# Kernel optimization log

Hardware: AMD Instinct MI355X
Metric: run time of the kernel (lower is better)

## Reference

```python
import jax, jax.numpy as jnp
import numpy as np

N = 8192
F_DIM = 512
H_DIM = 256


def _xavier(key, shape):
    fan_in, fan_out = shape
    limit = float(np.sqrt(6.0 / (fan_in + fan_out)))
    return jax.random.uniform(key, shape, jnp.float32, -limit, limit)


def setup_inputs() -> dict:
    key = jax.random.key(0)
    k1, k2, k3, k4, k5, k6, k7 = jax.random.split(key, 7)
    inp = {
        "input": jax.random.normal(k1, (N, F_DIM), jnp.float32),
        "wavelets": jax.random.normal(k2, (N, N), jnp.float32) / np.sqrt(N),
        "wavelets_inv": jax.random.normal(k3, (N, N), jnp.float32) / np.sqrt(N),
        "W1": _xavier(k4, (F_DIM, H_DIM)),
        "W2": _xavier(k5, (H_DIM, H_DIM)),
        "filter1": jax.random.uniform(k6, (N,), jnp.float32, 0.9, 1.1),
        "filter2": jax.random.uniform(k7, (N,), jnp.float32, 0.9, 1.1),
    }
    return inp


def _gwnn_layer(x, wavelets, wavelets_inv, weight, filt):
    # torch: wavelets @ diag(filt) @ (wavelets_inv @ (x @ W))
    # diag(filt) right-multiply == column-wise scale of wavelets (same math,
    # avoids the O(N^3) dense diag matmul).
    t = x @ weight                      # [N, C_out]
    s = wavelets_inv @ t                # [N, C_out] (spectral domain)
    return (wavelets * filt[None, :]) @ s  # [N, C_out]


def reference(input, wavelets, wavelets_inv, W1, W2, filter1, filter2):
    # eval mode: dropout is identity
    h1 = jax.nn.relu(_gwnn_layer(input, wavelets, wavelets_inv, W1, filter1))
    out = _gwnn_layer(h1, wavelets, wavelets_inv, W2, filter2)
    return out
```

## Files before the change

kernel.cpp:

```cpp
#include <hip/hip_runtime.h>
#include <hip/hip_bf16.h>

using f32x4 = __attribute__((ext_vector_type(4))) float;
using s16x8 = __attribute__((ext_vector_type(8))) short;

#define DEVFN static __device__ __forceinline__

static constexpr int NCOL = 256;
static constexpr int MROWS = 8192;
static constexpr int BM = 64;
static constexpr int BK = 64;
static constexpr int THREADS = 512;
static constexpr int NTILE = MROWS / BM;
static constexpr size_t PSLICE = (size_t)MROWS * NCOL;

DEVFN unsigned short f2bf(float f) {
  union { float f; unsigned u; } x; x.f = f;
  unsigned u = x.u;
  u += 0x7fffu + ((u >> 16) & 1u);
  return (unsigned short)(u >> 16);
}

DEVFN float bf2f(unsigned short u) {
  union { unsigned u; float f; } x; x.u = (unsigned)u << 16; return x.f;
}

DEVFN s16x8 pack8(f32x4 v0, f32x4 v1) {
  union { s16x8 v; __hip_bfloat162 h[4]; } pk;
  pk.h[0] = __float22bfloat162_rn(float2{v0[0], v0[1]});
  pk.h[1] = __float22bfloat162_rn(float2{v0[2], v0[3]});
  pk.h[2] = __float22bfloat162_rn(float2{v1[0], v1[1]});
  pk.h[3] = __float22bfloat162_rn(float2{v1[2], v1[3]});
  return pk.v;
}

DEVFN void async16(void* lds, const void* g) {
  __builtin_amdgcn_global_load_lds((const __attribute__((address_space(1))) unsigned*)g,
                                   (__attribute__((address_space(3))) unsigned*)lds,
                                   16, 0, 0);
}


template<int KS>
__global__ __launch_bounds__(THREADS, 4)
void gemm_b(const unsigned short* __restrict__ Ablk, int Kfull,
            const unsigned short* __restrict__ Bp8,
            unsigned short* __restrict__ Pout)
{
  __shared__ __align__(16) unsigned short As[2][BM * BK];
  __shared__ __align__(16) unsigned short Bs[2][BK * NCOL];

  const int nwg = NTILE * KS, q = nwg / 8;
  const int logical = (blockIdx.x & 7) * q + (blockIdx.x >> 3);
  const int kh = logical / NTILE;
  const int tile = logical % NTILE;
  const int klen = Kfull / KS;
  const int nt = klen / BK;
  const int k0 = kh * klen;
  const int KT = Kfull >> 6;
  const int tid = threadIdx.x, lane = tid & 63;
  const int wm = (tid >> 6) >> 2;
  const int wn = (tid >> 6) & 3;
  const int lr = lane & 15, lg = lane >> 4;

  auto stage = [&](int buf, int t) {
    const unsigned short* asrc = Ablk + ((size_t)tile * KT + (k0 >> 6) + t) * 4096 + tid * 8;
    async16(&As[buf][tid * 8], asrc);
    const unsigned short* bsrc = Bp8 + (size_t)(k0 + t * BK) * NCOL + tid * 8;
#pragma unroll
    for (int o = 0; o < 4; ++o)
      async16(&Bs[buf][o * 4096 + tid * 8], bsrc + o * 4096);
  };

  f32x4 acc[2][4] = {};

  stage(0, 0);

  int cur = 0;
  for (int t = 0; t < nt; ++t) {
    if (t + 1 < nt) {
      stage(cur ^ 1, t + 1);
      asm volatile("s_waitcnt vmcnt(5)");
    } else {
      asm volatile("s_waitcnt vmcnt(0)");
    }
    __builtin_amdgcn_s_barrier();
    __builtin_amdgcn_sched_barrier(0);
#pragma unroll
    for (int s = 0; s < 2; ++s) {
      const int kc = s * 4 + lg;
      const int r0 = wm * 32 + lr, r1 = r0 + 16;
      s16x8 a0 = *(const s16x8*)&As[cur][r0 * 64 + ((kc ^ (r0 & 7)) << 3)];
      s16x8 a1 = *(const s16x8*)&As[cur][r1 * 64 + ((kc ^ (r1 & 7)) << 3)];
#pragma unroll
      for (int fn = 0; fn < 4; ++fn) {
        s16x8 b = *(const s16x8*)&Bs[cur][kc * 2048 + (wn * 64 + fn * 16 + lr) * 8];
        acc[0][fn] = __builtin_amdgcn_mfma_f32_16x16x32_bf16(a0, b, acc[0][fn], 0, 0, 0);
        acc[1][fn] = __builtin_amdgcn_mfma_f32_16x16x32_bf16(a1, b, acc[1][fn], 0, 0, 0);
      }
    }
    __builtin_amdgcn_s_barrier();
    cur ^= 1;
  }

  unsigned short* dst = Pout + (size_t)kh * PSLICE;
#pragma unroll
  for (int fm = 0; fm < 2; ++fm) {
    const int r0 = tile * BM + wm * 32 + fm * 16 + lg * 4;
#pragma unroll
    for (int fn = 0; fn < 4; ++fn) {
      const int col = wn * 64 + fn * 16 + lr;
      ushort4 u;
      u.x = f2bf(acc[fm][fn][0]); u.y = f2bf(acc[fm][fn][1]);
      u.z = f2bf(acc[fm][fn][2]); u.w = f2bf(acc[fm][fn][3]);
      *(ushort4*)&dst[((size_t)(r0 >> 3) * 256 + col) * 8 + (r0 & 7)] = u;
    }
  }
}


template<int KTSH>
__global__ void k_cvt_ablk(const float* __restrict__ W, unsigned short* __restrict__ outp) {
  const int K = 64 << KTSH;
  size_t gid = (size_t)blockIdx.x * blockDim.x + threadIdx.x;
  const int k8 = (int)(gid & 7);
  const size_t rr = gid >> 3;
  const int row = (int)(rr & 63);
  const size_t bt = rr >> 6;
  const int t = (int)(bt & ((1 << KTSH) - 1));
  const size_t T = bt >> KTSH;
  const float* p = W + (T * 64 + row) * (size_t)K + t * 64 + k8 * 8;
  s16x8 v = pack8(*(const f32x4*)p, *(const f32x4*)(p + 4));
  *(s16x8*)&outp[bt * 4096 + row * 64 + ((k8 ^ (row & 7)) << 3)] = v;
}

__global__ void k_convert_p8(const float* __restrict__ W, int K,
                             unsigned short* __restrict__ outp) {
  int tid = blockIdx.x * blockDim.x + threadIdx.x;
  if (tid >= K * NCOL / 4) return;
  int j = tid & (NCOL - 1);
  int i0 = (tid >> 8) << 2;
  unsigned short u[4];
#pragma unroll
  for (int r = 0; r < 4; ++r) u[r] = f2bf(W[(size_t)(i0 + r) * NCOL + j]);
  size_t off = ((size_t)(i0 >> 3) * NCOL + j) * 8 + (i0 & 7);
  *(ushort4*)&outp[off] = make_ushort4(u[0], u[1], u[2], u[3]);
}

template<int MODE>
__global__ void k_reduce(const unsigned short* __restrict__ P,
                         const float* __restrict__ filt, void* __restrict__ Out) {
  const int tid = blockIdx.x * blockDim.x + threadIdx.x;
  const int j = tid & 255;
  const int i8 = tid >> 8;
  const int i0 = i8 * 8;
  const size_t base = ((size_t)i8 * 256 + j) * 8;
  s16x8 p0 = *(const s16x8*)&P[base];
  s16x8 p1 = *(const s16x8*)&P[base + PSLICE];
  s16x8 p2 = *(const s16x8*)&P[base + 2 * PSLICE];
  s16x8 p3 = *(const s16x8*)&P[base + 3 * PSLICE];
  float f[8];
#pragma unroll
  for (int r = 0; r < 8; ++r)
    f[r] = bf2f((unsigned short)p0[r]) + bf2f((unsigned short)p1[r])
         + bf2f((unsigned short)p2[r]) + bf2f((unsigned short)p3[r]);
  if constexpr (MODE == 0) {
    if (filt) {
#pragma unroll
      for (int r = 0; r < 8; ++r) f[r] *= filt[i0 + r];
    }
    union { s16x8 v; unsigned short u[8]; } o;
#pragma unroll
    for (int r = 0; r < 8; ++r) o.u[r] = f2bf(f[r]);
    *(s16x8*)&((unsigned short*)Out)[base] = o.v;
  } else if constexpr (MODE == 1) {
    unsigned short* O = (unsigned short*)Out;
#pragma unroll
    for (int r = 0; r < 8; ++r) {
      const int row = i0 + r;
      O[((size_t)(row >> 6) * 4 + (j >> 6)) * 4096 + (row & 63) * 64
        + ((((j >> 3) & 7) ^ (row & 7)) << 3) + (j & 7)] = f2bf(fmaxf(f[r], 0.f));
    }
  } else {
    float* O = (float*)Out;
#pragma unroll
    for (int r = 0; r < 8; ++r)
      O[(size_t)(i0 + r) * NCOL + j] = f[r];
  }
}

extern "C" void kernel_launch(void* const* d_in, const int* in_sizes, int n_in,
                              void* d_out, int out_size, void* d_ws, size_t ws_size,
                              hipStream_t stream) {
  const float* input = (const float*)d_in[0];
  const float* Wv    = (const float*)d_in[1];
  const float* Winv  = (const float*)d_in[2];
  const float* W1    = (const float*)d_in[3];
  const float* W2    = (const float*)d_in[4];
  const float* f1    = (const float*)d_in[5];
  const float* f2    = (const float*)d_in[6];
  float* out = (float*)d_out;

  char* ws = (char*)d_ws;
  unsigned short* WvB   = (unsigned short*)(ws);
  unsigned short* WinvB = (unsigned short*)(ws + 0x8000000);
  unsigned short* inB   = (unsigned short*)(ws + 0x10000000);
  unsigned short* partB = (unsigned short*)(ws + 0x10800000);
  unsigned short* t1p   = (unsigned short*)(ws + 0x11800000);
  unsigned short* s1p   = (unsigned short*)(ws + 0x11C00000);
  unsigned short* t2p   = (unsigned short*)(ws + 0x12000000);
  unsigned short* s2p   = (unsigned short*)(ws + 0x12400000);
  unsigned short* h1b   = (unsigned short*)(ws + 0x12800000);
  unsigned short* W1p   = (unsigned short*)(ws + 0x12C00000);
  unsigned short* W2p   = (unsigned short*)(ws + 0x12C40000);

  dim3 gT(THREADS);
  dim3 g4(NTILE * 4), g1(NTILE);
  dim3 rT(256), rG(MROWS * NCOL / 8 / 256);

  k_cvt_ablk<7><<<dim3(32768), rT, 0, stream>>>(Wv, WvB);
  k_cvt_ablk<7><<<dim3(32768), rT, 0, stream>>>(Winv, WinvB);
  k_cvt_ablk<3><<<dim3(2048),  rT, 0, stream>>>(input, inB);
  k_convert_p8<<<dim3(128), rT, 0, stream>>>(W1, 512, W1p);
  k_convert_p8<<<dim3(64),  rT, 0, stream>>>(W2, 256, W2p);

  gemm_b<1><<<g1, gT, 0, stream>>>(inB, 512, W1p, t1p);
  gemm_b<4><<<g4, gT, 0, stream>>>(WinvB, 8192, t1p, partB);
  k_reduce<0><<<rG, rT, 0, stream>>>(partB, f1, s1p);
  gemm_b<4><<<g4, gT, 0, stream>>>(WvB, 8192, s1p, partB);
  k_reduce<1><<<rG, rT, 0, stream>>>(partB, nullptr, h1b);
  gemm_b<1><<<g1, gT, 0, stream>>>(h1b, 256, W2p, t2p);
  gemm_b<4><<<g4, gT, 0, stream>>>(WinvB, 8192, t2p, partB);
  k_reduce<0><<<rG, rT, 0, stream>>>(partB, f2, s2p);
  gemm_b<4><<<g4, gT, 0, stream>>>(WvB, 8192, s2p, partB);
  k_reduce<2><<<rG, rT, 0, stream>>>(partB, nullptr, out);
}
```

Before: 386.6 us.

## Fuse fp32-to-bf16 conversion of wavelet matrices into first-layer GEMMs with writeback

Removes the standalone conversion kernels for the wavelet matrices and the input. The first-layer GEMMs load fp32 A tiles, pack them to bf16 in registers, store them to LDS, and write the bf16 tile to the workspace for reuse by the second layer. This avoids one full extra read of each large matrix but replaces async LDS loads with register-staged loads in those GEMMs. The A LDS layout is changed to a k-chunk-major layout without XOR swizzle, which may introduce bank conflicts.

```diff
diff --git a/kernel.cpp b/kernel.cpp
--- a/kernel.cpp
+++ b/kernel.cpp
@@ -41,14 +41,15 @@
 }
 
 
-template<int KS>
+template<bool AF32, bool WB, int KS>
 __global__ __launch_bounds__(THREADS, 4)
-void gemm_b(const unsigned short* __restrict__ Ablk, int Kfull,
+void gemm_f(const void* __restrict__ Aany, int Kfull,
             const unsigned short* __restrict__ Bp8,
-            unsigned short* __restrict__ Pout)
+            unsigned short* __restrict__ Pout,
+            unsigned short* __restrict__ Awb)
 {
-  __shared__ __align__(16) unsigned short As[2][BM * BK];
-  __shared__ __align__(16) unsigned short Bs[2][BK * NCOL];
+  __shared__ __align__(16) unsigned short As[2][4096];
+  __shared__ __align__(16) unsigned short Bs[2][16384];
 
   const int nwg = NTILE * KS, q = nwg / 8;
   const int logical = (blockIdx.x & 7) * q + (blockIdx.x >> 3);
@@ -58,46 +59,84 @@
   const int nt = klen / BK;
   const int k0 = kh * klen;
   const int KT = Kfull >> 6;
+  const int kt0 = k0 >> 6;
   const int tid = threadIdx.x, lane = tid & 63;
   const int wm = (tid >> 6) >> 2;
   const int wn = (tid >> 6) & 3;
   const int lr = lane & 15, lg = lane >> 4;
-
-  auto stage = [&](int buf, int t) {
-    const unsigned short* asrc = Ablk + ((size_t)tile * KT + (k0 >> 6) + t) * 4096 + tid * 8;
-    async16(&As[buf][tid * 8], asrc);
-    const unsigned short* bsrc = Bp8 + (size_t)(k0 + t * BK) * NCOL + tid * 8;
+  const int srow = tid >> 3, sk8 = tid & 7;
+
+  auto stageB = [&](int buf, int t) {
+    const unsigned short* b = Bp8 + (size_t)(k0 + t * BK) * 256 + tid * 8;
 #pragma unroll
     for (int o = 0; o < 4; ++o)
-      async16(&Bs[buf][o * 4096 + tid * 8], bsrc + o * 4096);
+      async16(&Bs[buf][o * 4096 + tid * 8], b + o * 4096);
+  };
+  auto stageA_bf = [&](int buf, int t) {
+    async16(&As[buf][tid * 8],
+            (const unsigned short*)Aany + ((size_t)tile * KT + kt0 + t) * 4096 + tid * 8);
+  };
+
+  f32x4 ra0, ra1;
+  auto loadA = [&](int t) {
+    const float* p = (const float*)Aany + (size_t)(tile * BM + srow) * Kfull
+                   + k0 + t * BK + sk8 * 8;
+    ra0 = *(const f32x4*)p; ra1 = *(const f32x4*)(p + 4);
+  };
+  auto putA = [&](int buf, int t) {
+    s16x8 v = pack8(ra0, ra1);
+    *(s16x8*)&As[buf][sk8 * 512 + srow * 8] = v;
+    if constexpr (WB)
+      *(s16x8*)&Awb[((size_t)tile * KT + kt0 + t) * 4096 + sk8 * 512 + srow * 8] = v;
   };
 
   f32x4 acc[2][4] = {};
 
-  stage(0, 0);
+  if constexpr (AF32) {
+    loadA(0); stageB(0, 0); putA(0, 0);
+    asm volatile("s_waitcnt lgkmcnt(0)");
+  } else {
+    stageA_bf(0, 0); stageB(0, 0);
+  }
 
   int cur = 0;
   for (int t = 0; t < nt; ++t) {
-    if (t + 1 < nt) {
-      stage(cur ^ 1, t + 1);
-      asm volatile("s_waitcnt vmcnt(5)");
+    if constexpr (AF32) {
+      if (t + 1 < nt) {
+        loadA(t + 1);
+        stageB(cur ^ 1, t + 1);
+        if constexpr (WB) asm volatile("s_waitcnt vmcnt(7)");
+        else              asm volatile("s_waitcnt vmcnt(6)");
+      } else {
+        asm volatile("s_waitcnt vmcnt(0)");
+      }
     } else {
-      asm volatile("s_waitcnt vmcnt(0)");
+      if (t + 1 < nt) {
+        stageA_bf(cur ^ 1, t + 1); stageB(cur ^ 1, t + 1);
+        asm volatile("s_waitcnt vmcnt(5)");
+      } else {
+        asm volatile("s_waitcnt vmcnt(0)");
+      }
     }
     __builtin_amdgcn_s_barrier();
     __builtin_amdgcn_sched_barrier(0);
 #pragma unroll
     for (int s = 0; s < 2; ++s) {
       const int kc = s * 4 + lg;
-      const int r0 = wm * 32 + lr, r1 = r0 + 16;
-      s16x8 a0 = *(const s16x8*)&As[cur][r0 * 64 + ((kc ^ (r0 & 7)) << 3)];
-      s16x8 a1 = *(const s16x8*)&As[cur][r1 * 64 + ((kc ^ (r1 & 7)) << 3)];
+      s16x8 a0 = *(const s16x8*)&As[cur][kc * 512 + (wm * 32 + lr) * 8];
+      s16x8 a1 = *(const s16x8*)&As[cur][kc * 512 + (wm * 32 + 16 + lr) * 8];
 #pragma unroll
       for (int fn = 0; fn < 4; ++fn) {
         s16x8 b = *(const s16x8*)&Bs[cur][kc * 2048 + (wn * 64 + fn * 16 + lr) * 8];
         acc[0][fn] = __builtin_amdgcn_mfma_f32_16x16x32_bf16(a0, b, acc[0][fn], 0, 0, 0);
         acc[1][fn] = __builtin_amdgcn_mfma_f32_16x16x32_bf16(a1, b, acc[1][fn], 0, 0, 0);
       }
+    }
+    if constexpr (AF32) {
+      __builtin_amdgcn_sched_barrier(0);
+      if (t + 1 < nt) putA(cur ^ 1, t + 1);
+      asm volatile("s_waitcnt lgkmcnt(0)");
+      __builtin_amdgcn_sched_barrier(0);
     }
     __builtin_amdgcn_s_barrier();
     cur ^= 1;
@@ -118,21 +157,6 @@
   }
 }
 
-
-template<int KTSH>
-__global__ void k_cvt_ablk(const float* __restrict__ W, unsigned short* __restrict__ outp) {
-  const int K = 64 << KTSH;
-  size_t gid = (size_t)blockIdx.x * blockDim.x + threadIdx.x;
-  const int k8 = (int)(gid & 7);
-  const size_t rr = gid >> 3;
-  const int row = (int)(rr & 63);
-  const size_t bt = rr >> 6;
-  const int t = (int)(bt & ((1 << KTSH) - 1));
-  const size_t T = bt >> KTSH;
-  const float* p = W + (T * 64 + row) * (size_t)K + t * 64 + k8 * 8;
-  s16x8 v = pack8(*(const f32x4*)p, *(const f32x4*)(p + 4));
-  *(s16x8*)&outp[bt * 4096 + row * 64 + ((k8 ^ (row & 7)) << 3)] = v;
-}
 
 __global__ void k_convert_p8(const float* __restrict__ W, int K,
                              unsigned short* __restrict__ outp) {
@@ -155,15 +179,13 @@
   const int i8 = tid >> 8;
   const int i0 = i8 * 8;
   const size_t base = ((size_t)i8 * 256 + j) * 8;
-  s16x8 p0 = *(const s16x8*)&P[base];
-  s16x8 p1 = *(const s16x8*)&P[base + PSLICE];
-  s16x8 p2 = *(const s16x8*)&P[base + 2 * PSLICE];
-  s16x8 p3 = *(const s16x8*)&P[base + 3 * PSLICE];
-  float f[8];
-#pragma unroll
-  for (int r = 0; r < 8; ++r)
-    f[r] = bf2f((unsigned short)p0[r]) + bf2f((unsigned short)p1[r])
-         + bf2f((unsigned short)p2[r]) + bf2f((unsigned short)p3[r]);
+  float f[8] = {};
+#pragma unroll
+  for (int h = 0; h < 4; ++h) {
+    s16x8 pv = *(const s16x8*)&P[base + (size_t)h * PSLICE];
+#pragma unroll
+    for (int r = 0; r < 8; ++r) f[r] += bf2f((unsigned short)pv[r]);
+  }
   if constexpr (MODE == 0) {
     if (filt) {
 #pragma unroll
@@ -178,8 +200,8 @@
 #pragma unroll
     for (int r = 0; r < 8; ++r) {
       const int row = i0 + r;
-      O[((size_t)(row >> 6) * 4 + (j >> 6)) * 4096 + (row & 63) * 64
-        + ((((j >> 3) & 7) ^ (row & 7)) << 3) + (j & 7)] = f2bf(fmaxf(f[r], 0.f));
+      O[((size_t)(row >> 6) * 4 + (j >> 6)) * 4096 + ((j >> 3) & 7) * 512
+        + (row & 63) * 8 + (j & 7)] = f2bf(fmaxf(f[r], 0.f));
     }
   } else {
     float* O = (float*)Out;
@@ -204,34 +226,36 @@
   char* ws = (char*)d_ws;
   unsigned short* WvB   = (unsigned short*)(ws);
   unsigned short* WinvB = (unsigned short*)(ws + 0x8000000);
-  unsigned short* inB   = (unsigned short*)(ws + 0x10000000);
-  unsigned short* partB = (unsigned short*)(ws + 0x10800000);
-  unsigned short* t1p   = (unsigned short*)(ws + 0x11800000);
-  unsigned short* s1p   = (unsigned short*)(ws + 0x11C00000);
-  unsigned short* t2p   = (unsigned short*)(ws + 0x12000000);
-  unsigned short* s2p   = (unsigned short*)(ws + 0x12400000);
-  unsigned short* h1b   = (unsigned short*)(ws + 0x12800000);
-  unsigned short* W1p   = (unsigned short*)(ws + 0x12C00000);
-  unsigned short* W2p   = (unsigned short*)(ws + 0x12C40000);
+  unsigned short* partB = (unsigned short*)(ws + 0x10000000);
+  unsigned short* t1p   = (unsigned short*)(ws + 0x11000000);
+  unsigned short* s1p   = (unsigned short*)(ws + 0x11400000);
+  unsigned short* t2p   = (unsigned short*)(ws + 0x11800000);
+  unsigned short* s2p   = (unsigned short*)(ws + 0x11C00000);
+  unsigned short* h1b   = (unsigned short*)(ws + 0x12000000);
+  unsigned short* W1p   = (unsigned short*)(ws + 0x12400000);
+  unsigned short* W2p   = (unsigned short*)(ws + 0x12440000);
 
   dim3 gT(THREADS);
   dim3 g4(NTILE * 4), g1(NTILE);
   dim3 rT(256), rG(MROWS * NCOL / 8 / 256);
 
-  k_cvt_ablk<7><<<dim3(32768), rT, 0, stream>>>(Wv, WvB);
-  k_cvt_ablk<7><<<dim3(32768), rT, 0, stream>>>(Winv, WinvB);
-  k_cvt_ablk<3><<<dim3(2048),  rT, 0, stream>>>(input, inB);
   k_convert_p8<<<dim3(128), rT, 0, stream>>>(W1, 512, W1p);
   k_convert_p8<<<dim3(64),  rT, 0, stream>>>(W2, 256, W2p);
 
-  gemm_b<1><<<g1, gT, 0, stream>>>(inB, 512, W1p, t1p);
-  gemm_b<4><<<g4, gT, 0, stream>>>(WinvB, 8192, t1p, partB);
+  gemm_f<true, false, 1><<<g1, gT, 0, stream>>>(
+      (const void*)input, 512, W1p, t1p, nullptr);
+  gemm_f<true, true, 4><<<g4, gT, 0, stream>>>(
+      (const void*)Winv, 8192, t1p, partB, WinvB);
   k_reduce<0><<<rG, rT, 0, stream>>>(partB, f1, s1p);
-  gemm_b<4><<<g4, gT, 0, stream>>>(WvB, 8192, s1p, partB);
+  gemm_f<true, true, 4><<<g4, gT, 0, stream>>>(
+      (const void*)Wv, 8192, s1p, partB, WvB);
   k_reduce<1><<<rG, rT, 0, stream>>>(partB, nullptr, h1b);
-  gemm_b<1><<<g1, gT, 0, stream>>>(h1b, 256, W2p, t2p);
-  gemm_b<4><<<g4, gT, 0, stream>>>(WinvB, 8192, t2p, partB);
+  gemm_f<false, false, 1><<<g1, gT, 0, stream>>>(
+      (const void*)h1b, 256, W2p, t2p, nullptr);
+  gemm_f<false, false, 4><<<g4, gT, 0, stream>>>(
+      (const void*)WinvB, 8192, t2p, partB, nullptr);
   k_reduce<0><<<rG, rT, 0, stream>>>(partB, f2, s2p);
-  gemm_b<4><<<g4, gT, 0, stream>>>(WvB, 8192, s2p, partB);
+  gemm_f<false, false, 4><<<g4, gT, 0, stream>>>(
+      (const void*)WvB, 8192, s2p, partB, nullptr);
   k_reduce<2><<<rG, rT, 0, stream>>>(partB, nullptr, out);
 }
```

Measured after the change: 364.2 us. 1.06x faster.
